# Optimization experiments

Measured on AMD Instinct MI355X. Metric: run time of the kernel, lower is better.

The kernel has to match this reference:

```python
import jax, jax.numpy as jnp
import numpy as np

B, N, F = 16, 250000, 500000  # batch, vertices, triangle faces


def setup_inputs() -> dict:
    key = jax.random.key(0)
    k1, k2 = jax.random.split(key)
    vert = jax.random.normal(k1, (B, N, 3), dtype=jnp.float32)
    faces = jax.random.randint(k2, (F, 3), 0, N)  # int32 triangle indices
    return {"vert": vert, "faces": faces}


def _edge_list(faces):
    # Each triangle (a,b,c) contributes undirected edges (a,b),(b,c),(c,a);
    # directed both ways: vertex a receives neighbors b,c; b receives a,c; c receives a,b.
    a, b, c = faces[:, 0], faces[:, 1], faces[:, 2]
    dst = jnp.concatenate([a, a, b, b, c, c])  # [6F] receiving vertex
    src = jnp.concatenate([b, c, a, c, a, b])  # [6F] neighbor vertex
    return src, dst


def reference(vert, faces):
    n = vert.shape[1]
    src, dst = _edge_list(faces)

    # degree per vertex (duplicate edges from shared faces are summed, matching
    # a coalesced sparse adjacency built from face edge lists)
    deg = jax.ops.segment_sum(jnp.ones_like(src, dtype=vert.dtype), dst,
                              num_segments=n)  # [N]

    # gather neighbor coordinates along edges, scatter-add into receiving vertex
    gathered = vert[:, src, :]  # [B, 6F, 3] -- dominant memory traffic
    neigh_sum = jax.vmap(
        lambda g: jax.ops.segment_sum(g, dst, num_segments=n))(gathered)  # [B,N,3]

    # uniform Laplacian: mean of neighbors minus the vertex itself
    lap = neigh_sum / jnp.maximum(deg, 1.0)[None, :, None] - vert  # [B,N,3]

    # per-vertex mean-curvature proxy: L2 norm over xyz (vert_ref=None branch)
    curve = jnp.sqrt(jnp.sum(lap * lap, axis=-1))  # [B,N]
    return curve
```

## Files before the change

### kernel.cpp

```cpp
#include <hip/hip_runtime.h>

static constexpr int B = 16;
static constexpr int N = 250000;
static constexpr int F = 500000;
static constexpr int C3 = 3 * F;
static constexpr int E = 6 * F;
static constexpr int RW = 48;
static constexpr int CAP = 24;
static constexpr int DS  = 16;

static constexpr size_t D_VT  = 0;
static constexpr size_t D_DEG = (size_t)N * RW * 2;
static constexpr size_t D_ADJ = D_DEG + (size_t)N * DS * 4;
static constexpr size_t D_NEED = D_ADJ + (size_t)N * CAP * 8;

static constexpr size_t C_VT  = 0;
static constexpr size_t C_ADJ = (size_t)N * RW * 2;
static constexpr size_t C_DEG = C_ADJ + (size_t)E * sizeof(int);
static constexpr size_t C_CNT = C_DEG + (size_t)N * sizeof(unsigned);
static constexpr size_t C_STA = C_CNT + 256;
static constexpr size_t C_RNK = C_STA + (size_t)N * sizeof(unsigned);

__device__ __forceinline__ unsigned short f2bf(float f) {
    unsigned u = __float_as_uint(f);
    return (unsigned short)((u + 0x7FFFu + ((u >> 16) & 1u)) >> 16);
}


__global__ __launch_bounds__(256) void uls_setup_direct(
    const float* __restrict__ vert, const int* __restrict__ faces,
    unsigned short* __restrict__ vt, unsigned* __restrict__ degp,
    long long* __restrict__ adjp)
{
    __shared__ unsigned short lus[16 * RW];
    int t = threadIdx.x;
    int n0 = blockIdx.x * 16;
    int b = t >> 4, v = t & 15;

    int e = blockIdx.x * 256 + t;
    bool e_ok = (e < C3);
    int f = e / 3;
    int c = e - 3 * f;
    int dst = 0, p0 = 0, p1 = 0;
    unsigned rv = 0;
    if (e_ok) {
        int a  = faces[3 * f + 0];
        int bb = faces[3 * f + 1];
        int cc = faces[3 * f + 2];
        dst = (c == 0) ? a : (c == 1) ? bb : cc;
        p0  = (c == 0) ? bb : a;
        p1  = (c == 2) ? bb : cc;
        rv = atomicAdd(&degp[(size_t)dst * DS], 2u);
    }

    const float* s = vert + (size_t)b * (N * 3) + (size_t)(n0 + v) * 3;
    lus[v * RW + 0 * 16 + b] = f2bf(s[0]);
    lus[v * RW + 1 * 16 + b] = f2bf(s[1]);
    lus[v * RW + 2 * 16 + b] = f2bf(s[2]);
    __syncthreads();
    const uint2* lu2 = (const uint2*)lus;
    uint2* d2 = (uint2*)(vt + (size_t)n0 * RW);
    if (t < 192) d2[t] = lu2[t];

    if (e_ok) {
        unsigned pi = rv >> 1;
        if (pi < (unsigned)CAP)
            adjp[(size_t)dst * CAP + pi] =
                (unsigned long long)(unsigned)p0 | ((unsigned long long)(unsigned)p1 << 32);
    }
}

__device__ __forceinline__ void acc_row(const unsigned short* __restrict__ r,
                                        int q, float (&acc)[3][4]) {
#pragma unroll
    for (int cc = 0; cc < 3; ++cc) {
        uint2 u = *(const uint2*)(r + cc * 16 + 4 * q);
        acc[cc][0] += __uint_as_float(u.x << 16);
        acc[cc][1] += __uint_as_float(u.x & 0xFFFF0000u);
        acc[cc][2] += __uint_as_float(u.y << 16);
        acc[cc][3] += __uint_as_float(u.y & 0xFFFF0000u);
    }
}

__global__ __launch_bounds__(256) void uls_gather_direct(
    const unsigned short* __restrict__ vt, const int* __restrict__ adj,
    const unsigned* __restrict__ degp, float* __restrict__ out)
{
    __shared__ float lds[16 * 65];
    int t = threadIdx.x;
    int q = t & 3;
    int v = t >> 2;
    int n = blockIdx.x * 64 + v;
    bool n_ok = (n < N);

    unsigned d = n_ok ? degp[(size_t)n * DS] : 0u;
    if (d > 2u * CAP) d = 2u * CAP;
    const int* a0 = adj + (size_t)n * (CAP * 2);

    float acc[3][4] = {{0,0,0,0},{0,0,0,0},{0,0,0,0}};
    unsigned j = 0;
    for (; j + 4 <= d; j += 4) {
        int2 p0 = *(const int2*)(a0 + j);
        int2 p1 = *(const int2*)(a0 + j + 2);
        acc_row(vt + (size_t)p0.x * RW, q, acc);
        acc_row(vt + (size_t)p0.y * RW, q, acc);
        acc_row(vt + (size_t)p1.x * RW, q, acc);
        acc_row(vt + (size_t)p1.y * RW, q, acc);
    }
    if (j < d) {
        int2 p0 = *(const int2*)(a0 + j);
        acc_row(vt + (size_t)p0.x * RW, q, acc);
        acc_row(vt + (size_t)p0.y * RW, q, acc);
    }

    if (n_ok) {
        float self[3][4];
        const unsigned short* rs = vt + (size_t)n * RW;
#pragma unroll
        for (int cc = 0; cc < 3; ++cc) {
            uint2 u = *(const uint2*)(rs + cc * 16 + 4 * q);
            self[cc][0] = __uint_as_float(u.x << 16);
            self[cc][1] = __uint_as_float(u.x & 0xFFFF0000u);
            self[cc][2] = __uint_as_float(u.y << 16);
            self[cc][3] = __uint_as_float(u.y & 0xFFFF0000u);
        }
        float inv = 1.0f / fmaxf((float)d, 1.0f);
#pragma unroll
        for (int k = 0; k < 4; ++k) {
            float lx = acc[0][k] * inv - self[0][k];
            float ly = acc[1][k] * inv - self[1][k];
            float lz = acc[2][k] * inv - self[2][k];
            lds[(4 * q + k) * 65 + v] = sqrtf(lx * lx + ly * ly + lz * lz);
        }
    }
    __syncthreads();
    int vo = t & 63;
    int nn = blockIdx.x * 64 + vo;
    if (nn < N) {
#pragma unroll
        for (int k = 0; k < 4; ++k) {
            int bo = (t >> 6) + 4 * k;
            out[(size_t)bo * N + nn] = lds[bo * 65 + vo];
        }
    }
}


__global__ __launch_bounds__(256) void uls_setup_csr(
    const float* __restrict__ vert, const int* __restrict__ faces,
    unsigned short* __restrict__ vt, unsigned* __restrict__ deg,
    unsigned* __restrict__ rank)
{
    __shared__ unsigned short lus[16 * RW];
    int t = threadIdx.x;
    int n0 = blockIdx.x * 16;
    int b = t >> 4, v = t & 15;
    int e = blockIdx.x * 256 + t;
    unsigned rv = 0;
    bool e_ok = (e < C3);
    int dst = e_ok ? faces[e] : 0;
    if (e_ok) rv = atomicAdd(&deg[dst], 2u);
    const float* s = vert + (size_t)b * (N * 3) + (size_t)(n0 + v) * 3;
    lus[v * RW + 0 * 16 + b] = f2bf(s[0]);
    lus[v * RW + 1 * 16 + b] = f2bf(s[1]);
    lus[v * RW + 2 * 16 + b] = f2bf(s[2]);
    __syncthreads();
    const uint2* lu2 = (const uint2*)lus;
    uint2* d2 = (uint2*)(vt + (size_t)n0 * RW);
    if (t < 192) d2[t] = lu2[t];
    if (e_ok) rank[e] = rv;
}

__global__ __launch_bounds__(256) void uls_alloc(
    const unsigned* __restrict__ deg, unsigned* __restrict__ start,
    unsigned* __restrict__ counter)
{
    __shared__ unsigned s[256];
    __shared__ unsigned base;
    int t = threadIdx.x;
    int n = blockIdx.x * 256 + t;
    unsigned d = (n < N) ? deg[n] : 0u;
    s[t] = d;
    __syncthreads();
    for (int off = 1; off < 256; off <<= 1) {
        unsigned v = (t >= off) ? s[t - off] : 0u;
        __syncthreads();
        s[t] += v;
        __syncthreads();
    }
    if (t == 255) base = atomicAdd(counter, s[255]);
    __syncthreads();
    if (n < N) start[n] = base + (s[t] - d);
}

__global__ __launch_bounds__(256) void uls_fill(
    const int* __restrict__ faces, const unsigned* __restrict__ start,
    const unsigned* __restrict__ rank, int* __restrict__ adj)
{
    int e = blockIdx.x * 256 + threadIdx.x;
    if (e >= C3) return;
    int f = e / 3;
    int c = e - 3 * f;
    int a  = faces[3 * f + 0];
    int b  = faces[3 * f + 1];
    int cc = faces[3 * f + 2];
    int dst = (c == 0) ? a : (c == 1) ? b : cc;
    int p0  = (c == 0) ? b : a;
    int p1  = (c == 2) ? b : cc;
    unsigned p = start[dst] + rank[e];
    *(int2*)(adj + p) = make_int2(p0, p1);
}

__global__ __launch_bounds__(256) void uls_gather_csr(
    const unsigned short* __restrict__ vt, const int* __restrict__ adj,
    const unsigned* __restrict__ start, const unsigned* __restrict__ deg,
    float* __restrict__ out)
{
    __shared__ float lds[16 * 65];
    int t = threadIdx.x;
    int q = t & 3;
    int v = t >> 2;
    int n = blockIdx.x * 64 + v;
    bool n_ok = (n < N);
    unsigned d  = n_ok ? deg[n]   : 0u;
    unsigned s0 = n_ok ? start[n] : 0u;
    float acc[3][4] = {{0,0,0,0},{0,0,0,0},{0,0,0,0}};
    unsigned j = 0;
    for (; j + 4 <= d; j += 4) {
        int2 p0 = *(const int2*)(adj + s0 + j);
        int2 p1 = *(const int2*)(adj + s0 + j + 2);
        acc_row(vt + (size_t)p0.x * RW, q, acc);
        acc_row(vt + (size_t)p0.y * RW, q, acc);
        acc_row(vt + (size_t)p1.x * RW, q, acc);
        acc_row(vt + (size_t)p1.y * RW, q, acc);
    }
    if (j < d) {
        int2 p0 = *(const int2*)(adj + s0 + j);
        acc_row(vt + (size_t)p0.x * RW, q, acc);
        acc_row(vt + (size_t)p0.y * RW, q, acc);
    }
    if (n_ok) {
        float self[3][4];
        const unsigned short* rs = vt + (size_t)n * RW;
#pragma unroll
        for (int cc = 0; cc < 3; ++cc) {
            uint2 u = *(const uint2*)(rs + cc * 16 + 4 * q);
            self[cc][0] = __uint_as_float(u.x << 16);
            self[cc][1] = __uint_as_float(u.x & 0xFFFF0000u);
            self[cc][2] = __uint_as_float(u.y << 16);
            self[cc][3] = __uint_as_float(u.y & 0xFFFF0000u);
        }
        float inv = 1.0f / fmaxf((float)d, 1.0f);
#pragma unroll
        for (int k = 0; k < 4; ++k) {
            float lx = acc[0][k] * inv - self[0][k];
            float ly = acc[1][k] * inv - self[1][k];
            float lz = acc[2][k] * inv - self[2][k];
            lds[(4 * q + k) * 65 + v] = sqrtf(lx * lx + ly * ly + lz * lz);
        }
    }
    __syncthreads();
    int vo = t & 63;
    int nn = blockIdx.x * 64 + vo;
    if (nn < N) {
#pragma unroll
        for (int k = 0; k < 4; ++k) {
            int bo = (t >> 6) + 4 * k;
            out[(size_t)bo * N + nn] = lds[bo * 65 + vo];
        }
    }
}


extern "C" void kernel_launch(void* const* d_in, const int* in_sizes, int n_in,
                              void* d_out, int out_size, void* d_ws, size_t ws_size,
                              hipStream_t stream) {
    const float* vert  = (const float*)d_in[0];
    const int*   faces = (const int*)d_in[1];
    float* out = (float*)d_out;
    char* ws = (char*)d_ws;

    if (ws_size >= D_NEED) {
        unsigned short* vt   = (unsigned short*)(ws + D_VT);
        unsigned*       degp = (unsigned*)(ws + D_DEG);
        long long*      adj  = (long long*)(ws + D_ADJ);
        hipMemsetAsync(degp, 0, (size_t)N * DS * 4, stream);
        uls_setup_direct<<<N / 16, 256, 0, stream>>>(vert, faces, vt, degp, adj);
        uls_gather_direct<<<(N + 63) / 64, 256, 0, stream>>>(vt, (const int*)adj, degp, out);
    } else {
        unsigned short* vt      = (unsigned short*)(ws + C_VT);
        int*            adj     = (int*)(ws + C_ADJ);
        unsigned*       deg     = (unsigned*)(ws + C_DEG);
        unsigned*       counter = (unsigned*)(ws + C_CNT);
        unsigned*       start   = (unsigned*)(ws + C_STA);
        unsigned*       rank    = (unsigned*)(ws + C_RNK);
        hipMemsetAsync(ws + C_DEG, 0, (C_CNT + 256) - C_DEG, stream);
        uls_setup_csr<<<N / 16, 256, 0, stream>>>(vert, faces, vt, deg, rank);
        uls_alloc<<<(N + 255) / 256, 256, 0, stream>>>(deg, start, counter);
        uls_fill<<<(C3 + 255) / 256, 256, 0, stream>>>(faces, start, rank, adj);
        uls_gather_csr<<<(N + 63) / 64, 256, 0, stream>>>(vt, adj, start, deg, out);
    }
}
```

Measured before the change: 266.7 us.

## Slice setup atomics by vertex range and widen gather unroll to eight

The setup kernel now assigns one thread per face and replicates each face across 8 vertex-range slices. Each block only does the degree atomics and adjacency writes for vertices in its own slice, aiming for better locality of those scattered writes. The bf16 transpose stays on the first N/16 blocks. The gather kernel loads the self row earlier and walks the adjacency list eight entries at a time with int4 index loads, to expose more independent row loads. The cost is that every face is re-read 8 times, and adjacent blocks still touch all slices at the same time.

Result: faster. 257.1 us (-3.6%).

```diff
diff --git a/kernel.cpp b/kernel.cpp
--- a/kernel.cpp
+++ b/kernel.cpp
@@ -8,6 +8,9 @@
 static constexpr int RW = 48;
 static constexpr int CAP = 24;
 static constexpr int DS  = 16;
+static constexpr int SLICE = N / 8;
+static constexpr int SETUP_G = ((F + 255) / 256) * 8;
+static_assert(SETUP_G >= N / 16, "setup grid must still cover the transpose");
 
 static constexpr size_t D_VT  = 0;
 static constexpr size_t D_DEG = (size_t)N * RW * 2;
@@ -26,6 +29,11 @@
     return (unsigned short)((u + 0x7FFFu + ((u >> 16) & 1u)) >> 16);
 }
 
+__device__ __forceinline__ long long pack_pair(int p0, int p1) {
+    return (long long)((unsigned long long)(unsigned)p0 |
+                       ((unsigned long long)(unsigned)p1 << 32));
+}
+
 
 __global__ __launch_bounds__(256) void uls_setup_direct(
     const float* __restrict__ vert, const int* __restrict__ faces,
@@ -33,41 +41,47 @@
     long long* __restrict__ adjp)
 {
     __shared__ unsigned short lus[16 * RW];
-    int t = threadIdx.x;
-    int n0 = blockIdx.x * 16;
-    int b = t >> 4, v = t & 15;
-
-    int e = blockIdx.x * 256 + t;
-    bool e_ok = (e < C3);
-    int f = e / 3;
-    int c = e - 3 * f;
-    int dst = 0, p0 = 0, p1 = 0;
-    unsigned rv = 0;
-    if (e_ok) {
-        int a  = faces[3 * f + 0];
-        int bb = faces[3 * f + 1];
-        int cc = faces[3 * f + 2];
-        dst = (c == 0) ? a : (c == 1) ? bb : cc;
-        p0  = (c == 0) ? bb : a;
-        p1  = (c == 2) ? bb : cc;
-        rv = atomicAdd(&degp[(size_t)dst * DS], 2u);
-    }
-
-    const float* s = vert + (size_t)b * (N * 3) + (size_t)(n0 + v) * 3;
-    lus[v * RW + 0 * 16 + b] = f2bf(s[0]);
-    lus[v * RW + 1 * 16 + b] = f2bf(s[1]);
-    lus[v * RW + 2 * 16 + b] = f2bf(s[2]);
-    __syncthreads();
-    const uint2* lu2 = (const uint2*)lus;
-    uint2* d2 = (uint2*)(vt + (size_t)n0 * RW);
-    if (t < 192) d2[t] = lu2[t];
-
-    if (e_ok) {
-        unsigned pi = rv >> 1;
-        if (pi < (unsigned)CAP)
-            adjp[(size_t)dst * CAP + pi] =
-                (unsigned long long)(unsigned)p0 | ((unsigned long long)(unsigned)p1 << 32);
-    }
+    int t   = threadIdx.x;
+    int bid = blockIdx.x;
+    int s   = bid & 7;
+    int g   = bid >> 3;
+    int f   = g * 256 + t;
+    bool f_ok = (f < F);
+    unsigned lo = (unsigned)(s * SLICE);
+
+    int a = 0, b2 = 0, c2 = 0;
+    if (f_ok) {
+        a  = faces[3 * f + 0];
+        b2 = faces[3 * f + 1];
+        c2 = faces[3 * f + 2];
+    }
+    bool k0 = f_ok && ((unsigned)a  - lo < (unsigned)SLICE);
+    bool k1 = f_ok && ((unsigned)b2 - lo < (unsigned)SLICE);
+    bool k2 = f_ok && ((unsigned)c2 - lo < (unsigned)SLICE);
+    unsigned r0 = 0, r1 = 0, r2 = 0;
+    if (k0) r0 = atomicAdd(&degp[(size_t)a  * DS], 2u);
+    if (k1) r1 = atomicAdd(&degp[(size_t)b2 * DS], 2u);
+    if (k2) r2 = atomicAdd(&degp[(size_t)c2 * DS], 2u);
+
+    if (bid < N / 16) {
+        int n0 = bid * 16;
+        int bb = t >> 4, v = t & 15;
+        const float* sp = vert + (size_t)bb * (N * 3) + (size_t)(n0 + v) * 3;
+        lus[v * RW + 0 * 16 + bb] = f2bf(sp[0]);
+        lus[v * RW + 1 * 16 + bb] = f2bf(sp[1]);
+        lus[v * RW + 2 * 16 + bb] = f2bf(sp[2]);
+        __syncthreads();
+        const uint2* lu2 = (const uint2*)lus;
+        uint2* d2 = (uint2*)(vt + (size_t)n0 * RW);
+        if (t < 192) d2[t] = lu2[t];
+    }
+
+    if (k0) { unsigned pi = r0 >> 1; if (pi < (unsigned)CAP)
+        adjp[(size_t)a  * CAP + pi] = pack_pair(b2, c2); }
+    if (k1) { unsigned pi = r1 >> 1; if (pi < (unsigned)CAP)
+        adjp[(size_t)b2 * CAP + pi] = pack_pair(a, c2); }
+    if (k2) { unsigned pi = r2 >> 1; if (pi < (unsigned)CAP)
+        adjp[(size_t)c2 * CAP + pi] = pack_pair(a, b2); }
 }
 
 __device__ __forceinline__ void acc_row(const unsigned short* __restrict__ r,
@@ -97,24 +111,8 @@
     if (d > 2u * CAP) d = 2u * CAP;
     const int* a0 = adj + (size_t)n * (CAP * 2);
 
-    float acc[3][4] = {{0,0,0,0},{0,0,0,0},{0,0,0,0}};
-    unsigned j = 0;
-    for (; j + 4 <= d; j += 4) {
-        int2 p0 = *(const int2*)(a0 + j);
-        int2 p1 = *(const int2*)(a0 + j + 2);
-        acc_row(vt + (size_t)p0.x * RW, q, acc);
-        acc_row(vt + (size_t)p0.y * RW, q, acc);
-        acc_row(vt + (size_t)p1.x * RW, q, acc);
-        acc_row(vt + (size_t)p1.y * RW, q, acc);
-    }
-    if (j < d) {
-        int2 p0 = *(const int2*)(a0 + j);
-        acc_row(vt + (size_t)p0.x * RW, q, acc);
-        acc_row(vt + (size_t)p0.y * RW, q, acc);
-    }
-
+    float self[3][4] = {{0,0,0,0},{0,0,0,0},{0,0,0,0}};
     if (n_ok) {
-        float self[3][4];
         const unsigned short* rs = vt + (size_t)n * RW;
 #pragma unroll
         for (int cc = 0; cc < 3; ++cc) {
@@ -124,6 +122,37 @@
             self[cc][2] = __uint_as_float(u.y << 16);
             self[cc][3] = __uint_as_float(u.y & 0xFFFF0000u);
         }
+    }
+
+    float acc[3][4] = {{0,0,0,0},{0,0,0,0},{0,0,0,0}};
+    unsigned j = 0;
+    for (; j + 8 <= d; j += 8) {
+        int4 q0 = *(const int4*)(a0 + j);
+        int4 q1 = *(const int4*)(a0 + j + 4);
+        acc_row(vt + (size_t)q0.x * RW, q, acc);
+        acc_row(vt + (size_t)q0.y * RW, q, acc);
+        acc_row(vt + (size_t)q0.z * RW, q, acc);
+        acc_row(vt + (size_t)q0.w * RW, q, acc);
+        acc_row(vt + (size_t)q1.x * RW, q, acc);
+        acc_row(vt + (size_t)q1.y * RW, q, acc);
+        acc_row(vt + (size_t)q1.z * RW, q, acc);
+        acc_row(vt + (size_t)q1.w * RW, q, acc);
+    }
+    if (j + 4 <= d) {
+        int4 q0 = *(const int4*)(a0 + j);
+        acc_row(vt + (size_t)q0.x * RW, q, acc);
+        acc_row(vt + (size_t)q0.y * RW, q, acc);
+        acc_row(vt + (size_t)q0.z * RW, q, acc);
+        acc_row(vt + (size_t)q0.w * RW, q, acc);
+        j += 4;
+    }
+    if (j < d) {
+        int2 p0 = *(const int2*)(a0 + j);
+        acc_row(vt + (size_t)p0.x * RW, q, acc);
+        acc_row(vt + (size_t)p0.y * RW, q, acc);
+    }
+
+    if (n_ok) {
         float inv = 1.0f / fmaxf((float)d, 1.0f);
 #pragma unroll
         for (int k = 0; k < 4; ++k) {
@@ -285,7 +314,7 @@
         unsigned*       degp = (unsigned*)(ws + D_DEG);
         long long*      adj  = (long long*)(ws + D_ADJ);
         hipMemsetAsync(degp, 0, (size_t)N * DS * 4, stream);
-        uls_setup_direct<<<N / 16, 256, 0, stream>>>(vert, faces, vt, degp, adj);
+        uls_setup_direct<<<SETUP_G, 256, 0, stream>>>(vert, faces, vt, degp, adj);
         uls_gather_direct<<<(N + 63) / 64, 256, 0, stream>>>(vt, (const int*)adj, degp, out);
     } else {
         unsigned short* vt      = (unsigned short*)(ws + C_VT);
```
